# Performance work log

Measured on AMD Instinct MI355X. Metric: run time of the kernel, lower is better.

Reference implementation:

```python
import jax, jax.numpy as jnp
import numpy as np

B, S, E, H, MLP = 2, 2048, 1024, 16, 4096
VEC = 8          # args.vec_length: block-row height of vector-sparse mask
SPARSITY = 0.9   # fraction of attention entries dropped
D = E // H


def _make_mask():
    # static_random_mask_aligned: each block-row of VEC query rows keeps a
    # random ~(1-sparsity) subset of key columns. Diagonal kept so every
    # softmax row is non-empty.
    rng = np.random.default_rng(0)
    block = rng.random((S // VEC, S)) < (1.0 - SPARSITY)   # [m, n]
    mask = np.repeat(block, VEC, axis=0)                   # [S, S]
    mask |= np.eye(S, dtype=bool)
    return jnp.asarray(mask)


def setup_inputs() -> dict:
    key = jax.random.key(0)
    ks = jax.random.split(key, 8)
    w = lambda k, shp: (0.02 * jax.random.normal(k, shp, dtype=jnp.float32))
    return {
        "x": jax.random.normal(ks[0], (B, S, E), dtype=jnp.float32),
        "mask": _make_mask(),                       # [S,S] bool, static
        "w_qkv": w(ks[1], (3 * E, E)),             # in_proj_weight
        "b_qkv": jnp.zeros((3 * E,), jnp.float32),
        "w_out": w(ks[2], (E, E)),                 # out_proj
        "b_out": jnp.zeros((E,), jnp.float32),
        "g1": jnp.ones((E,), jnp.float32), "beta1": jnp.zeros((E,), jnp.float32),
        "g2": jnp.ones((E,), jnp.float32), "beta2": jnp.zeros((E,), jnp.float32),
        "w1": w(ks[3], (MLP, E)), "bias1": jnp.zeros((MLP,), jnp.float32),
        "w2": w(ks[4], (E, MLP)), "bias2": jnp.zeros((E,), jnp.float32),
    }


def _layer_norm(x, g, b, eps=1e-5):
    mu = jnp.mean(x, axis=-1, keepdims=True)
    var = jnp.mean(jnp.square(x - mu), axis=-1, keepdims=True)
    return (x - mu) * jax.lax.rsqrt(var + eps) * g + b


def _sparse_mha(h, mask, w_qkv, b_qkv, w_out, b_out):
    qkv = jnp.einsum("bse,fe->bsf", h, w_qkv) + b_qkv       # [B,S,3E]
    q, k, v = jnp.split(qkv, 3, axis=-1)
    q = q.reshape(B, S, H, D)
    k = k.reshape(B, S, H, D)
    v = v.reshape(B, S, H, D)
    scores = jnp.einsum("bqhd,bkhd->bhqk", q, k) / jnp.sqrt(jnp.float32(D))
    scores = jnp.where(mask[None, None], scores, jnp.float32(-1e9))
    p = jax.nn.softmax(scores, axis=-1)
    ctx = jnp.einsum("bhqk,bkhd->bqhd", p, v).reshape(B, S, E)
    return jnp.einsum("bse,fe->bsf", ctx, w_out) + b_out


def reference(x, mask, w_qkv, b_qkv, w_out, b_out, g1, beta1, g2, beta2,
              w1, bias1, w2, bias2):
    h = _layer_norm(x, g1, beta1)
    attn = _sparse_mha(h, mask, w_qkv, b_qkv, w_out, b_out)
    out = attn + x                      # residual 1
    out = _layer_norm(out, g2, beta2)
    out = jnp.einsum("bse,me->bsm", out, w1) + bias1   # linear1 (no activation, as in source)
    out = jnp.einsum("bsm,em->bse", out, w2) + bias2   # linear2
    return out + x                      # residual adds ORIGINAL x (as in source)
```

## Files before the change

kernel.cpp:

```cpp
#include <hip/hip_runtime.h>
#include <cstdint>
#include <cstddef>

typedef unsigned short u16;
typedef unsigned int u32;
typedef short s16x8 __attribute__((ext_vector_type(8)));
typedef float f32x4 __attribute__((ext_vector_type(4)));
typedef float v2f __attribute__((ext_vector_type(2)));
typedef _Float16 f16x2 __attribute__((ext_vector_type(2)));

__device__ __forceinline__ float fdot2(f16x2 a, f16x2 b, float c) {
#if defined(__HIP_DEVICE_COMPILE__) && __has_builtin(__builtin_amdgcn_fdot2)
  return __builtin_amdgcn_fdot2(a, b, c, false);
#else
  return (float)a.x * (float)b.x + (float)a.y * (float)b.y + c;
#endif
}

__device__ __forceinline__ float red8(float x) {
#if defined(__HIP_DEVICE_COMPILE__) && __has_builtin(__builtin_amdgcn_update_dpp)
  int xi = __float_as_int(x);
  x += __int_as_float(__builtin_amdgcn_update_dpp(0, xi, 0xB1, 0xF, 0xF, true));
  xi = __float_as_int(x);
  x += __int_as_float(__builtin_amdgcn_update_dpp(0, xi, 0x4E, 0xF, 0xF, true));
  xi = __float_as_int(x);
  x += __int_as_float(__builtin_amdgcn_update_dpp(0, xi, 0x141, 0xF, 0xF, true));
  return x;
#else
  x += __shfl_xor(x, 1); x += __shfl_xor(x, 2); x += __shfl_xor(x, 4);
  return x;
#endif
}

#define S_LEN 2048
#define EMB   1024
#define NHEAD 16
#define HD    64
#define E3    3072
#define MLPD  4096
#define NROWS 4096
#define LCAP  640

__device__ __forceinline__ float bf2f(u16 v) {
  union { u32 i; float f; } c; c.i = ((u32)v) << 16; return c.f;
}
__device__ __forceinline__ u16 f2bf(float f) {
  union { float f; u32 i; } c; c.f = f;
  u32 x = c.i;
  return (u16)((x + 0x7FFFu + ((x >> 16) & 1u)) >> 16);
}
__device__ __forceinline__ u16 f2h(float f) {
  _Float16 h = (_Float16)f;
  union { _Float16 h; u16 b; } c; c.h = h; return c.b;
}

__device__ __forceinline__ void gl2lds16(const void* g, void* l) {
  __builtin_amdgcn_global_load_lds(
      (__attribute__((address_space(1))) void*)(g),
      (__attribute__((address_space(3))) void*)(l), 16, 0, 0);
}

__global__ void detect_flags(const u32* __restrict__ w1s, int* __restrict__ dtflag,
                             const u32* __restrict__ mask, int* __restrict__ maskrep) {
  __shared__ int hits[256];
  __shared__ u32 red[256];
  int h = 0; u32 v = 0;
  for (int i = threadIdx.x; i < 4096; i += 256) {
    u32 w = w1s[i];
    if ((w & 0xFFFFu) && (((w >> 7) & 0xFFu) >= 0xC8u)) ++h;
    v |= mask[i];
  }
  hits[threadIdx.x] = h; red[threadIdx.x] = v;
  __syncthreads();
  if (threadIdx.x == 0) {
    int t = 0; u32 o = 0;
    for (int i = 0; i < 256; ++i) { t += hits[i]; o |= red[i]; }
    *dtflag = (t > 8) ? 1 : 0;
    int rep;
    if (o <= 1u) rep = 0;
    else if (o & 0x80u) rep = 1;
    else if (o & 0x00800000u) rep = 2;
    else rep = 3;
    *maskrep = rep;
  }
}

__device__ __forceinline__ bool maskbit(const void* m, int rep, size_t idx) {
  switch (rep) {
    case 0:  return ((const int*)m)[idx] != 0;
    case 1:  return ((const u16*)m)[idx] != 0;
    case 2:  return ((const u32*)m)[idx] != 0;
    default: return ((const unsigned char*)m)[idx] != 0;
  }
}

__global__ __launch_bounds__(256)
void cvt_kernel(const void* __restrict__ src, u16* __restrict__ dst,
                int n8, const int* __restrict__ dtflag) {
  const int i = blockIdx.x * blockDim.x + threadIdx.x;
  if (i >= n8) return;
  if (*dtflag) {
    const float4 a = ((const float4*)src)[i * 2];
    const float4 b = ((const float4*)src)[i * 2 + 1];
    u16 o[8] = {f2bf(a.x), f2bf(a.y), f2bf(a.z), f2bf(a.w),
                f2bf(b.x), f2bf(b.y), f2bf(b.z), f2bf(b.w)};
    *(uint4*)(dst + (size_t)i * 8) = *(const uint4*)o;
  } else {
    ((uint4*)dst)[i] = ((const uint4*)src)[i];
  }
}

__global__ void cvt_small(const void* s0, u16* d0, const void* s1, u16* d1,
                          const void* s2, u16* d2, const void* s3, u16* d3,
                          const void* s4, u16* d4, const void* s5, u16* d5,
                          const void* s6, u16* d6, const void* s7, u16* d7,
                          const int* __restrict__ dtflag) {
  const int f = *dtflag;
  const void* srcs[8] = {s0, s1, s2, s3, s4, s5, s6, s7};
  u16* dsts[8] = {d0, d1, d2, d3, d4, d5, d6, d7};
  const int ns[8] = {E3, EMB, EMB, EMB, EMB, EMB, MLPD, EMB};
#pragma unroll
  for (int k = 0; k < 8; ++k) {
    for (int idx = threadIdx.x; idx < ns[k]; idx += 256)
      dsts[k][idx] = f ? f2bf(((const float*)srcs[k])[idx])
                       : ((const u16*)srcs[k])[idx];
  }
}

__global__ void build_lists(const void* __restrict__ mask, const int* __restrict__ repf,
                            int* __restrict__ lists, int* __restrict__ cnt,
                            unsigned char* __restrict__ diagflag) {
  __shared__ int num;
  const int m = blockIdx.x;
  if (threadIdx.x == 0) num = 0;
  __syncthreads();
  const int rep = *repf;
  const int row0 = m * 8;
  for (int j = threadIdx.x; j < S_LEN; j += 256) {
    int srcrow = (j == row0) ? (row0 + 1) : row0;
    bool bit = maskbit(mask, rep, (size_t)srcrow * S_LEN + j);
    if (j >= row0 && j < row0 + 8) diagflag[j] = bit ? 0 : 1;
    if (bit) {
      int p = atomicAdd(&num, 1);
      if (p < LCAP) lists[m * LCAP + p] = j * 2048;
    }
  }
  __syncthreads();
  if (threadIdx.x == 0) cnt[m] = (num < LCAP) ? num : LCAP;
}

__global__ __launch_bounds__(256)
void ln_kernel(const void* __restrict__ Xv, const u16* __restrict__ g,
               const u16* __restrict__ be, u16* __restrict__ O,
               const int* __restrict__ inf32) {
  const int wv = threadIdx.x >> 6, ln = threadIdx.x & 63;
  const int row = blockIdx.x * 4 + wv;
  float v[16];
  if (inf32 && *inf32) {
    const float* xr = (const float*)Xv + (size_t)row * EMB;
    float4 a0 = *(const float4*)(xr + ln * 8);
    float4 a1 = *(const float4*)(xr + ln * 8 + 4);
    float4 b0 = *(const float4*)(xr + 512 + ln * 8);
    float4 b1 = *(const float4*)(xr + 512 + ln * 8 + 4);
    v[0]=a0.x; v[1]=a0.y; v[2]=a0.z; v[3]=a0.w; v[4]=a1.x; v[5]=a1.y; v[6]=a1.z; v[7]=a1.w;
    v[8]=b0.x; v[9]=b0.y; v[10]=b0.z; v[11]=b0.w; v[12]=b1.x; v[13]=b1.y; v[14]=b1.z; v[15]=b1.w;
  } else {
    const u16* xr = (const u16*)Xv + (size_t)row * EMB;
    union { uint4 u; u16 s[8]; } p0, p1;
    p0.u = *(const uint4*)(xr + ln * 8);
    p1.u = *(const uint4*)(xr + 512 + ln * 8);
#pragma unroll
    for (int t = 0; t < 8; ++t) { v[t] = bf2f(p0.s[t]); v[8 + t] = bf2f(p1.s[t]); }
  }
  float s = 0.f, sq = 0.f;
#pragma unroll
  for (int t = 0; t < 16; ++t) { s += v[t]; sq += v[t] * v[t]; }
#pragma unroll
  for (int off = 32; off; off >>= 1) { s += __shfl_xor(s, off); sq += __shfl_xor(sq, off); }
  const float mu = s * (1.0f / EMB);
  const float var = sq * (1.0f / EMB) - mu * mu;
  const float rsig = rsqrtf(var + 1e-5f);
  union { uint4 u; u16 s[8]; } g0, g1v, b0, b1v, o0, o1;
  g0.u = *(const uint4*)(g + ln * 8);   g1v.u = *(const uint4*)(g + 512 + ln * 8);
  b0.u = *(const uint4*)(be + ln * 8);  b1v.u = *(const uint4*)(be + 512 + ln * 8);
#pragma unroll
  for (int t = 0; t < 8; ++t) {
    o0.s[t] = f2bf((v[t]     - mu) * rsig * bf2f(g0.s[t])  + bf2f(b0.s[t]));
    o1.s[t] = f2bf((v[8 + t] - mu) * rsig * bf2f(g1v.s[t]) + bf2f(b1v.s[t]));
  }
  u16* orow = O + (size_t)row * EMB;
  *(uint4*)(orow + ln * 8) = o0.u;
  *(uint4*)(orow + 512 + ln * 8) = o1.u;
}

__global__ __launch_bounds__(256)
void gemm_bt(const u16* __restrict__ A, const u16* __restrict__ B,
             const u16* __restrict__ bias, u16* __restrict__ C,
             int M, int N, int K) {
  __shared__ u16 a_sh[128 * 64];
  __shared__ u16 b_sh[128 * 64];
  const int tid = threadIdx.x;
  const int wv = tid >> 6, ln = tid & 63;
  const int wm = wv & 1, wn = wv >> 1;
  const int tm = blockIdx.y, tn = blockIdx.x;
  const int srow = ln >> 3;
  const int scol = ((ln & 7) ^ srow) * 8;
  const int q = ln >> 4, rr = ln & 15;

  f32x4 acc[4][4] = {};
  const u16* Abase = A + (size_t)(tm * 128) * K;
  const u16* Bbase = B + (size_t)(tn * 128) * K;

  for (int k0 = 0; k0 < K; k0 += 64) {
    __syncthreads();
#pragma unroll
    for (int c = 0; c < 4; ++c) {
      const int chunk = wv * 4 + c;
      const int row = chunk * 8 + srow;
      gl2lds16(Abase + (size_t)row * K + k0 + scol, &a_sh[chunk * 512]);
      gl2lds16(Bbase + (size_t)row * K + k0 + scol, &b_sh[chunk * 512]);
    }
    __syncthreads();
#pragma unroll
    for (int kk = 0; kk < 2; ++kk) {
      const int slot = ((kk * 4 + q) ^ (rr & 7)) * 8;
      s16x8 af[4], bfr[4];
#pragma unroll
      for (int mi = 0; mi < 4; ++mi)
        af[mi] = *(const s16x8*)&a_sh[(wm * 64 + mi * 16 + rr) * 64 + slot];
#pragma unroll
      for (int ni = 0; ni < 4; ++ni)
        bfr[ni] = *(const s16x8*)&b_sh[(wn * 64 + ni * 16 + rr) * 64 + slot];
#pragma unroll
      for (int mi = 0; mi < 4; ++mi)
#pragma unroll
        for (int ni = 0; ni < 4; ++ni)
          acc[mi][ni] = __builtin_amdgcn_mfma_f32_16x16x32_bf16(af[mi], bfr[ni], acc[mi][ni], 0, 0, 0);
    }
  }
#pragma unroll
  for (int ni = 0; ni < 4; ++ni) {
    const int col = tn * 128 + wn * 64 + ni * 16 + rr;
    const float bv = bf2f(bias[col]);
#pragma unroll
    for (int mi = 0; mi < 4; ++mi)
#pragma unroll
      for (int r2 = 0; r2 < 4; ++r2) {
        const int row = tm * 128 + wm * 64 + mi * 16 + q * 4 + r2;
        C[(size_t)row * N + col] = f2bf(acc[mi][ni][r2] + bv);
      }
  }
}

__global__ __launch_bounds__(256)
void gemm_qkv(const u16* __restrict__ A, const u16* __restrict__ B,
              const u16* __restrict__ bias,
              u16* __restrict__ Qb, u16* __restrict__ Kp, u16* __restrict__ Vp,
              int K) {
  __shared__ u16 a_sh[128 * 64];
  __shared__ u16 b_sh[128 * 64];
  const int tid = threadIdx.x;
  const int wv = tid >> 6, ln = tid & 63;
  const int wm = wv & 1, wn = wv >> 1;
  const int tm = blockIdx.y, tn = blockIdx.x;
  const int srow = ln >> 3;
  const int scol = ((ln & 7) ^ srow) * 8;
  const int q = ln >> 4, rr = ln & 15;

  f32x4 acc[4][4] = {};
  const u16* Abase = A + (size_t)(tm * 128) * K;
  const u16* Bbase = B + (size_t)(tn * 128) * K;

  for (int k0 = 0; k0 < K; k0 += 64) {
    __syncthreads();
#pragma unroll
    for (int c = 0; c < 4; ++c) {
      const int chunk = wv * 4 + c;
      const int row = chunk * 8 + srow;
      gl2lds16(Abase + (size_t)row * K + k0 + scol, &a_sh[chunk * 512]);
      gl2lds16(Bbase + (size_t)row * K + k0 + scol, &b_sh[chunk * 512]);
    }
    __syncthreads();
#pragma unroll
    for (int kk = 0; kk < 2; ++kk) {
      const int slot = ((kk * 4 + q) ^ (rr & 7)) * 8;
      s16x8 af[4], bfr[4];
#pragma unroll
      for (int mi = 0; mi < 4; ++mi)
        af[mi] = *(const s16x8*)&a_sh[(wm * 64 + mi * 16 + rr) * 64 + slot];
#pragma unroll
      for (int ni = 0; ni < 4; ++ni)
        bfr[ni] = *(const s16x8*)&b_sh[(wn * 64 + ni * 16 + rr) * 64 + slot];
#pragma unroll
      for (int mi = 0; mi < 4; ++mi)
#pragma unroll
        for (int ni = 0; ni < 4; ++ni)
          acc[mi][ni] = __builtin_amdgcn_mfma_f32_16x16x32_bf16(af[mi], bfr[ni], acc[mi][ni], 0, 0, 0);
    }
  }
  const int third = (tn * 128) >> 10;
#pragma unroll
  for (int ni = 0; ni < 4; ++ni) {
    const int col = tn * 128 + wn * 64 + ni * 16 + rr;
    const int w = col & 1023;
    const float bv = bf2f(bias[col]);
#pragma unroll
    for (int mi = 0; mi < 4; ++mi)
#pragma unroll
      for (int r2 = 0; r2 < 4; ++r2) {
        const int row = tm * 128 + wm * 64 + mi * 16 + q * 4 + r2;
        const float o = acc[mi][ni][r2] + bv;
        const size_t idx = (size_t)row * 1024 + w;
        if (third == 0)      Qb[idx] = f2bf(o);
        else if (third == 1) Kp[idx] = f2h(o);
        else                 Vp[idx] = f2bf(o);
      }
  }
}

__global__ __launch_bounds__(256)
void gemm_bt_n64(const u16* __restrict__ A, const u16* __restrict__ B,
                 const u16* __restrict__ bias, const void* __restrict__ resid,
                 void* __restrict__ Cv, int M, int N, int K,
                 const int* __restrict__ residf32, const int* __restrict__ outf32) {
  __shared__ u16 a_sh[128 * 64];
  __shared__ u16 b_sh[64 * 64];
  const int tid = threadIdx.x;
  const int wv = tid >> 6, ln = tid & 63;
  const int wm = wv & 1, wn = wv >> 1;
  const int tm = blockIdx.y, tn = blockIdx.x;
  const int srow = ln >> 3;
  const int scol = ((ln & 7) ^ srow) * 8;
  const int q = ln >> 4, rr = ln & 15;

  f32x4 acc[4][2] = {};
  const u16* Abase = A + (size_t)(tm * 128) * K;
  const u16* Bbase = B + (size_t)(tn * 64) * K;

  for (int k0 = 0; k0 < K; k0 += 64) {
    __syncthreads();
#pragma unroll
    for (int c = 0; c < 4; ++c) {
      const int chunk = wv * 4 + c;
      const int row = chunk * 8 + srow;
      gl2lds16(Abase + (size_t)row * K + k0 + scol, &a_sh[chunk * 512]);
    }
#pragma unroll
    for (int c = 0; c < 2; ++c) {
      const int chunk = wv * 2 + c;
      const int row = chunk * 8 + srow;
      gl2lds16(Bbase + (size_t)row * K + k0 + scol, &b_sh[chunk * 512]);
    }
    __syncthreads();
#pragma unroll
    for (int kk = 0; kk < 2; ++kk) {
      const int slot = ((kk * 4 + q) ^ (rr & 7)) * 8;
      s16x8 af[4], bfr[2];
#pragma unroll
      for (int mi = 0; mi < 4; ++mi)
        af[mi] = *(const s16x8*)&a_sh[(wm * 64 + mi * 16 + rr) * 64 + slot];
#pragma unroll
      for (int ni = 0; ni < 2; ++ni)
        bfr[ni] = *(const s16x8*)&b_sh[(wn * 32 + ni * 16 + rr) * 64 + slot];
#pragma unroll
      for (int mi = 0; mi < 4; ++mi)
#pragma unroll
        for (int ni = 0; ni < 2; ++ni)
          acc[mi][ni] = __builtin_amdgcn_mfma_f32_16x16x32_bf16(af[mi], bfr[ni], acc[mi][ni], 0, 0, 0);
    }
  }
  const int rf32 = residf32 ? *residf32 : 0;
  const int f32o = outf32 ? *outf32 : 0;
#pragma unroll
  for (int ni = 0; ni < 2; ++ni) {
    const int col = tn * 64 + wn * 32 + ni * 16 + rr;
    const float bv = bf2f(bias[col]);
#pragma unroll
    for (int mi = 0; mi < 4; ++mi)
#pragma unroll
      for (int r2 = 0; r2 < 4; ++r2) {
        const int row = tm * 128 + wm * 64 + mi * 16 + q * 4 + r2;
        const size_t idx = (size_t)row * N + col;
        float o = acc[mi][ni][r2] + bv;
        if (resid)
          o += rf32 ? ((const float*)resid)[idx] : bf2f(((const u16*)resid)[idx]);
        if (f32o) ((float*)Cv)[idx] = o;
        else      ((u16*)Cv)[idx] = f2bf(o);
      }
  }
}

__global__ __launch_bounds__(512)
void attn_kernel(const u16* __restrict__ Qb, const u16* __restrict__ Kp,
                 const u16* __restrict__ Vp, const int* __restrict__ lists,
                 const int* __restrict__ cnt, const unsigned char* __restrict__ diagflag,
                 u16* __restrict__ ctx) {
  __shared__ int list_sh[LCAP];
  const int g = blockIdx.x;
  const int b = g >> 12;
  const int h = (g >> 8) & 15;
  const int m = g & 255;
  const int tid = threadIdx.x, wv = tid >> 6, ln = tid & 63;
  const int es = ln >> 3, dc = ln & 7;
  const int i = m * 8 + wv;
  const int n = cnt[m];

  for (int e = tid; e < n; e += 512) list_sh[e] = lists[m * LCAP + e];
  __syncthreads();

  const u16* qrow = Qb + (size_t)(b * S_LEN + i) * EMB + h * 64 + dc * 8;
  union { uint4 u; u16 s[8]; } qi; qi.u = *(const uint4*)qrow;
  f16x2 q2[4];
#pragma unroll
  for (int t = 0; t < 4; ++t) {
    q2[t].x = (_Float16)(bf2f(qi.s[2 * t])     * 0.125f);
    q2[t].y = (_Float16)(bf2f(qi.s[2 * t + 1]) * 0.125f);
  }

  const char* kbase = (const char*)Kp + (size_t)b * S_LEN * 2048 + h * 128 + dc * 16;
  const char* vbase = (const char*)Vp + (size_t)b * S_LEN * 2048 + h * 128 + dc * 16;

  float sum = 0.f;
  v2f acc2[4] = {};

  auto score = [&](const uint4& ku) -> float {
    union { uint4 u; f16x2 p[4]; } kk; kk.u = ku;
    float s = fdot2(kk.p[3], q2[3], fdot2(kk.p[2], q2[2],
              fdot2(kk.p[1], q2[1], fdot2(kk.p[0], q2[0], 0.f))));
    s = red8(s);
    return __expf(fminf(fmaxf(s, -60.f), 60.f));
  };
  auto doV = [&](const uint4& vu, float p) {
    const u32 r[4] = {vu.x, vu.y, vu.z, vu.w};
    v2f pv; pv.x = p; pv.y = p;
#pragma unroll
    for (int t = 0; t < 4; ++t) {
      union { u32 i; float f; } lo, hi;
      lo.i = r[t] << 16; hi.i = r[t] & 0xFFFF0000u;
      v2f w; w.x = lo.f; w.y = hi.f;
      acc2[t] += pv * w;
    }
  };

  const int df = diagflag[i];
  if (df) {
    const int dioff = i * 2048;
    const uint4 ku = *(const uint4*)(kbase + dioff);
    const uint4 vu = *(const uint4*)(vbase + dioff);
    float p = score(ku);
    p = (es == 0) ? p : 0.f;
    sum += p;
    doV(vu, p);
  }

  int e0 = 0;
  for (; e0 + 16 <= n; e0 += 16) {
    const int offA = list_sh[e0 + es];
    const int offB = list_sh[e0 + 8 + es];
    const uint4 kA = *(const uint4*)(kbase + (size_t)offA);
    const uint4 kB = *(const uint4*)(kbase + (size_t)offB);
    const uint4 vA = *(const uint4*)(vbase + (size_t)offA);
    const uint4 vB = *(const uint4*)(vbase + (size_t)offB);
    const float pA = score(kA);
    const float pB = score(kB);
    sum += pA + pB;
    doV(vA, pA);
    doV(vB, pB);
  }
  for (; e0 + 8 <= n; e0 += 8) {
    const int off = list_sh[e0 + es];
    const uint4 ku = *(const uint4*)(kbase + (size_t)off);
    const uint4 vu = *(const uint4*)(vbase + (size_t)off);
    const float p = score(ku);
    sum += p;
    doV(vu, p);
  }
  if (e0 < n) {
    const int e = e0 + es;
    const bool valid = (e < n);
    const int off = valid ? list_sh[e] : list_sh[0];
    const uint4 ku = *(const uint4*)(kbase + (size_t)off);
    const uint4 vu = *(const uint4*)(vbase + (size_t)off);
    float p = score(ku);
    p = valid ? p : 0.f;
    sum += p;
    doV(vu, p);
  }

#pragma unroll
  for (int off = 8; off < 64; off <<= 1) {
    sum += __shfl_xor(sum, off);
#pragma unroll
    for (int t = 0; t < 4; ++t) {
      acc2[t].x += __shfl_xor(acc2[t].x, off);
      acc2[t].y += __shfl_xor(acc2[t].y, off);
    }
  }

  if (es == 0) {
    const float inv = 1.0f / sum;
    u16 o[8];
#pragma unroll
    for (int t = 0; t < 4; ++t) {
      o[2 * t]     = f2bf(acc2[t].x * inv);
      o[2 * t + 1] = f2bf(acc2[t].y * inv);
    }
    *(uint4*)(ctx + (size_t)(b * S_LEN + i) * EMB + h * 64 + dc * 8) = *(const uint4*)o;
  }
}

extern "C" void kernel_launch(void* const* d_in, const int* in_sizes, int n_in,
                              void* d_out, int out_size, void* d_ws, size_t ws_size,
                              hipStream_t stream) {
  const void* x_raw    = d_in[0];
  const void* mask     = d_in[1];
  const void* wqkv_raw = d_in[2];
  const void* bqkv_raw = d_in[3];
  const void* wout_raw = d_in[4];
  const void* bout_raw = d_in[5];
  const void* g1_raw   = d_in[6];
  const void* be1_raw  = d_in[7];
  const void* g2_raw   = d_in[8];
  const void* be2_raw  = d_in[9];
  const void* w1_raw   = d_in[10];
  const void* b1_raw   = d_in[11];
  const void* w2_raw   = d_in[12];
  const void* b2_raw   = d_in[13];

  char* ws = (char*)d_ws;
  const size_t MB = 1u << 20;
  int* dtflag         = (int*)ws;
  int* maskrep        = (int*)(ws + 64);
  int* cnt            = (int*)(ws + 1024);
  unsigned char* dfl  = (unsigned char*)(ws + 4096);
  int* lists          = (int*)(ws + 8192);
  u16* R1  = (u16*)(ws + 1 * MB);
  u16* Qb  = (u16*)(ws + 9 * MB);
  u16* Kp  = (u16*)(ws + 17 * MB);
  u16* Vp  = (u16*)(ws + 25 * MB);
  u16* M1  = (u16*)(ws + 17 * MB);
  u16* W   = (u16*)(ws + 49 * MB);
  char* sm = ws + 57 * MB;
  u16* bq  = (u16*)(sm);
  u16* bo  = (u16*)(sm + 8192);
  u16* g1b = (u16*)(sm + 16384);
  u16* be1b= (u16*)(sm + 24576);
  u16* g2b = (u16*)(sm + 32768);
  u16* be2b= (u16*)(sm + 40960);
  u16* b1b = (u16*)(sm + 49152);
  u16* b2b = (u16*)(sm + 65536);

  detect_flags<<<dim3(1), dim3(256), 0, stream>>>((const u32*)w1_raw, dtflag,
                                                  (const u32*)mask, maskrep);
  build_lists<<<dim3(256), dim3(256), 0, stream>>>(mask, maskrep, lists, cnt, dfl);
  cvt_small<<<dim3(1), dim3(256), 0, stream>>>(
      bqkv_raw, bq, bout_raw, bo, g1_raw, g1b, be1_raw, be1b,
      g2_raw, g2b, be2_raw, be2b, b1_raw, b1b, b2_raw, b2b, dtflag);

  auto cvt = [&](const void* src, u16* dst, int n) {
    const int n8 = n / 8;
    cvt_kernel<<<dim3((n8 + 255) / 256), dim3(256), 0, stream>>>(src, dst, n8, dtflag);
  };

  ln_kernel<<<dim3(NROWS / 4), dim3(256), 0, stream>>>(x_raw, g1b, be1b, R1, dtflag);
  cvt(wqkv_raw, W, E3 * EMB);
  gemm_qkv<<<dim3(E3 / 128, NROWS / 128), dim3(256), 0, stream>>>(
      R1, W, bq, Qb, Kp, Vp, EMB);
  attn_kernel<<<dim3(2 * NHEAD * 256), dim3(512), 0, stream>>>(
      Qb, Kp, Vp, lists, cnt, dfl, R1);
  cvt(wout_raw, W, EMB * EMB);
  gemm_bt_n64<<<dim3(EMB / 64, NROWS / 128), dim3(256), 0, stream>>>(
      R1, W, bo, x_raw, Qb, NROWS, EMB, EMB, dtflag, nullptr);
  ln_kernel<<<dim3(NROWS / 4), dim3(256), 0, stream>>>(Qb, g2b, be2b, R1, nullptr);
  cvt(w1_raw, W, MLPD * EMB);
  gemm_bt<<<dim3(MLPD / 128, NROWS / 128), dim3(256), 0, stream>>>(
      R1, W, b1b, M1, NROWS, MLPD, EMB);
  cvt(w2_raw, W, EMB * MLPD);
  gemm_bt_n64<<<dim3(EMB / 64, NROWS / 128), dim3(256), 0, stream>>>(
      M1, W, b2b, x_raw, d_out, NROWS, EMB, MLPD, dtflag, dtflag);
}
```

Measured before the change: 487.7 us.

## Split-K the final MLP down-projection GEMM with a separate combine kernel

Replaces the 64-wide-tile linear2 GEMM with a 128x128 tile GEMM that splits K=4096 into two halves across blockIdx.z, writing bf16 partial results into two scratch buffers. A new combine kernel sums the partials, adds the bias and the original residual x, and writes the output in fp32 or bf16. The intent is to keep the block count up while using larger tiles for more data reuse. The cost is an extra kernel launch, extra memory traffic for the partials, and an added bf16 rounding of each partial sum.

```diff
diff --git a/kernel.cpp b/kernel.cpp
--- a/kernel.cpp
+++ b/kernel.cpp
@@ -249,6 +249,99 @@
         const int row = tm * 128 + wm * 64 + mi * 16 + q * 4 + r2;
         C[(size_t)row * N + col] = f2bf(acc[mi][ni][r2] + bv);
       }
+  }
+}
+
+__global__ __launch_bounds__(256)
+void gemm_bt_sk(const u16* __restrict__ A, const u16* __restrict__ B,
+                u16* __restrict__ P0, u16* __restrict__ P1,
+                int M, int N, int K) {
+  __shared__ u16 a_sh[128 * 64];
+  __shared__ u16 b_sh[128 * 64];
+  const int tid = threadIdx.x;
+  const int wv = tid >> 6, ln = tid & 63;
+  const int wm = wv & 1, wn = wv >> 1;
+  const int tm = blockIdx.y, tn = blockIdx.x, kz = blockIdx.z;
+  const int Kh = K >> 1;
+  const int koff = kz * Kh;
+  const int srow = ln >> 3;
+  const int scol = ((ln & 7) ^ srow) * 8;
+  const int q = ln >> 4, rr = ln & 15;
+
+  f32x4 acc[4][4] = {};
+  const u16* Abase = A + (size_t)(tm * 128) * K + koff;
+  const u16* Bbase = B + (size_t)(tn * 128) * K + koff;
+
+  for (int k0 = 0; k0 < Kh; k0 += 64) {
+    __syncthreads();
+#pragma unroll
+    for (int c = 0; c < 4; ++c) {
+      const int chunk = wv * 4 + c;
+      const int row = chunk * 8 + srow;
+      gl2lds16(Abase + (size_t)row * K + k0 + scol, &a_sh[chunk * 512]);
+      gl2lds16(Bbase + (size_t)row * K + k0 + scol, &b_sh[chunk * 512]);
+    }
+    __syncthreads();
+#pragma unroll
+    for (int kk = 0; kk < 2; ++kk) {
+      const int slot = ((kk * 4 + q) ^ (rr & 7)) * 8;
+      s16x8 af[4], bfr[4];
+#pragma unroll
+      for (int mi = 0; mi < 4; ++mi)
+        af[mi] = *(const s16x8*)&a_sh[(wm * 64 + mi * 16 + rr) * 64 + slot];
+#pragma unroll
+      for (int ni = 0; ni < 4; ++ni)
+        bfr[ni] = *(const s16x8*)&b_sh[(wn * 64 + ni * 16 + rr) * 64 + slot];
+#pragma unroll
+      for (int mi = 0; mi < 4; ++mi)
+#pragma unroll
+        for (int ni = 0; ni < 4; ++ni)
+          acc[mi][ni] = __builtin_amdgcn_mfma_f32_16x16x32_bf16(af[mi], bfr[ni], acc[mi][ni], 0, 0, 0);
+    }
+  }
+  u16* P = kz ? P1 : P0;
+#pragma unroll
+  for (int ni = 0; ni < 4; ++ni) {
+    const int col = tn * 128 + wn * 64 + ni * 16 + rr;
+#pragma unroll
+    for (int mi = 0; mi < 4; ++mi)
+#pragma unroll
+      for (int r2 = 0; r2 < 4; ++r2) {
+        const int row = tm * 128 + wm * 64 + mi * 16 + q * 4 + r2;
+        P[(size_t)row * N + col] = f2bf(acc[mi][ni][r2]);
+      }
+  }
+}
+
+__global__ __launch_bounds__(256)
+void combine_kernel(const u16* __restrict__ P0, const u16* __restrict__ P1,
+                    const u16* __restrict__ bias, const void* __restrict__ xr,
+                    void* __restrict__ Ov, const int* __restrict__ f32io) {
+  const int i = blockIdx.x * 256 + threadIdx.x;
+  const int col8 = (i & 127) * 8;
+  union { uint4 u; u16 s[8]; } a, b, bi;
+  a.u = ((const uint4*)P0)[i];
+  b.u = ((const uint4*)P1)[i];
+  bi.u = *(const uint4*)(bias + col8);
+  const int f = *f32io;
+  float o[8];
+#pragma unroll
+  for (int t = 0; t < 8; ++t) o[t] = bf2f(a.s[t]) + bf2f(b.s[t]) + bf2f(bi.s[t]);
+  if (f) {
+    const float4 x0 = ((const float4*)xr)[i * 2];
+    const float4 x1 = ((const float4*)xr)[i * 2 + 1];
+    o[0]+=x0.x; o[1]+=x0.y; o[2]+=x0.z; o[3]+=x0.w;
+    o[4]+=x1.x; o[5]+=x1.y; o[6]+=x1.z; o[7]+=x1.w;
+    float4 r0 = {o[0],o[1],o[2],o[3]}, r1 = {o[4],o[5],o[6],o[7]};
+    ((float4*)Ov)[i * 2] = r0;
+    ((float4*)Ov)[i * 2 + 1] = r1;
+  } else {
+    union { uint4 u; u16 s[8]; } xv;
+    xv.u = ((const uint4*)xr)[i];
+    u16 r[8];
+#pragma unroll
+    for (int t = 0; t < 8; ++t) r[t] = f2bf(o[t] + bf2f(xv.s[t]));
+    ((uint4*)Ov)[i] = *(const uint4*)r;
   }
 }
 
@@ -576,6 +669,8 @@
   gemm_bt<<<dim3(MLPD / 128, NROWS / 128), dim3(256), 0, stream>>>(
       R1, W, b1b, M1, NROWS, MLPD, EMB);
   cvt(w2_raw, W, EMB * MLPD);
-  gemm_bt_n64<<<dim3(EMB / 64, NROWS / 128), dim3(256), 0, stream>>>(
-      M1, W, b2b, x_raw, d_out, NROWS, EMB, MLPD, dtflag, dtflag);
-}
+  gemm_bt_sk<<<dim3(EMB / 128, NROWS / 128, 2), dim3(256), 0, stream>>>(
+      M1, W, R1, Qb, NROWS, EMB, MLPD);
+  combine_kernel<<<dim3(NROWS * EMB / 8 / 256), dim3(256), 0, stream>>>(
+      R1, Qb, b2b, x_raw, d_out, dtflag);
+}
```

New measurement: 453.9 us. -6.9%, faster.
